# Kernel tuning notes

Hardware: AMD Instinct MI355X
Metric: run time of the kernel (lower is better)

The kernel has to match this reference:

```python
import jax, jax.numpy as jnp
import numpy as np

B, S, D = 2, 2048, 2048
H = 16
HD = D // H  # 128
ROPE_BASE = 10000.0


def _rope_cos_sin(seq_len, head_dim):
    inv_freq = 1.0 / (ROPE_BASE ** (jnp.arange(0, head_dim, 2, dtype=jnp.float32) / head_dim))
    t = jnp.arange(seq_len, dtype=jnp.float32)
    freqs = jnp.einsum('i,j->ij', t, inv_freq)  # [S, HD/2]
    emb = jnp.concatenate([freqs, freqs], axis=-1)  # [S, HD]
    return jnp.cos(emb)[None, None], jnp.sin(emb)[None, None]  # [1,1,S,HD]


def _rotate_half(x):
    x1, x2 = jnp.split(x, 2, axis=-1)
    return jnp.concatenate([-x2, x1], axis=-1)


def setup_inputs() -> dict:
    key = jax.random.key(0)
    k1, k2, k3 = jax.random.split(key, 3)
    hidden_states = jax.random.normal(k1, (B, S, D), dtype=jnp.float32)
    w_qkv = jax.random.normal(k2, (D, 3 * D), dtype=jnp.float32) * (D ** -0.5)
    w_o = jax.random.normal(k3, (D, D), dtype=jnp.float32) * (D ** -0.5)
    return {"hidden_states": hidden_states, "w_qkv": w_qkv, "w_o": w_o}


def reference(hidden_states, w_qkv, w_o):
    b, s, _ = hidden_states.shape
    qkv = jnp.einsum('bsd,de->bse', hidden_states, w_qkv)  # [B,S,3D]
    q, k, v = jnp.split(qkv, 3, axis=-1)
    # [B,H,S,HD]
    q = q.reshape(b, s, H, HD).transpose(0, 2, 1, 3)
    k = k.reshape(b, s, H, HD).transpose(0, 2, 1, 3)
    v = v.reshape(b, s, H, HD).transpose(0, 2, 1, 3)
    cos, sin = _rope_cos_sin(s, HD)
    q = q * cos + _rotate_half(q) * sin
    k = k * cos + _rotate_half(k) * sin
    scale = 1.0 / np.sqrt(HD).astype(np.float32)
    scores = jnp.einsum('bhqd,bhkd->bhqk', q, k) * scale  # [B,H,S,S]
    causal = jnp.triu(jnp.ones((s, s), dtype=bool), k=1)
    scores = jnp.where(causal, -jnp.inf, scores)
    attn = jax.nn.softmax(scores, axis=-1)
    out = jnp.einsum('bhqk,bhkd->bhqd', attn, v)  # [B,H,S,HD]
    out = out.transpose(0, 2, 1, 3).reshape(b, s, H * HD)
    return jnp.einsum('bsd,de->bse', out, w_o)
```

## Files before the change

kernel.cpp:

```cpp
#include <hip/hip_runtime.h>
#include <math.h>

typedef unsigned short u16;
typedef short s16x8 __attribute__((ext_vector_type(8)));
typedef float f32x4 __attribute__((ext_vector_type(4)));

#define ATTN_SCALE 0.08838834764831845f
#define NEG_BIG -1.0e30f

__device__ __forceinline__ u16 f2bf(float f) {
  union { float f; unsigned u; } c; c.f = f;
  return (u16)((c.u + 0x7fffu + ((c.u >> 16) & 1u)) >> 16);
}
__device__ __forceinline__ float bf2f(u16 v) {
  union { unsigned u; float f; } c; c.u = ((unsigned)v) << 16;
  return c.f;
}
__device__ __forceinline__ f32x4 mfma16(s16x8 a, s16x8 b, f32x4 c) {
  return __builtin_amdgcn_mfma_f32_16x16x32_bf16(a, b, c, 0, 0, 0);
}
__device__ __forceinline__ void gl_lds16(const u16* g, u16* l) {
  __builtin_amdgcn_global_load_lds(
      (const __attribute__((address_space(1))) unsigned int*)g,
      (__attribute__((address_space(3))) unsigned int*)l, 16, 0, 0);
}

__global__ __launch_bounds__(256) void k_cast(const float* __restrict__ in,
                                              u16* __restrict__ out, int n4) {
  const int i = blockIdx.x * 256 + threadIdx.x;
  if (i >= n4) return;
  const float4 v = ((const float4*)in)[i];
  ushort4 o;
  o.x = f2bf(v.x); o.y = f2bf(v.y); o.z = f2bf(v.z); o.w = f2bf(v.w);
  ((ushort4*)out)[i] = o;
}

__global__ __launch_bounds__(256) void k_transpose_cast(const float* __restrict__ in,
                                                        u16* __restrict__ out,
                                                        int R, int C) {
  __shared__ __attribute__((aligned(16))) u16 tile[32][33];
  const int c0 = blockIdx.x * 32, r0 = blockIdx.y * 32;
  const int tx = threadIdx.x, ty = threadIdx.y;
#pragma unroll
  for (int i = 0; i < 4; ++i)
    tile[ty + 8 * i][tx] = f2bf(in[(r0 + ty + 8 * i) * C + c0 + tx]);
  __syncthreads();
#pragma unroll
  for (int i = 0; i < 4; ++i)
    out[(c0 + ty + 8 * i) * R + r0 + tx] = tile[tx][ty + 8 * i];
}

__global__ __launch_bounds__(256) void k_vtrans(const u16* __restrict__ qkv,
                                                u16* __restrict__ vt) {
  __shared__ __attribute__((aligned(16))) u16 tile[32][33];
  const int bh = blockIdx.z, b = bh >> 4, h = bh & 15;
  const int s0 = blockIdx.x * 32, d0 = blockIdx.y * 32;
  const int tx = threadIdx.x, ty = threadIdx.y;
#pragma unroll
  for (int i = 0; i < 4; ++i) {
    const int s = s0 + ty + 8 * i;
    tile[ty + 8 * i][tx] = qkv[(b * 2048 + s) * 6144 + 4096 + h * 128 + d0 + tx];
  }
  __syncthreads();
#pragma unroll
  for (int i = 0; i < 4; ++i) {
    const int d = d0 + ty + 8 * i;
    vt[bh * 262144 + d * 2048 + s0 + tx] = tile[tx][ty + 8 * i];
  }
}

__global__ __launch_bounds__(256) void k_rope(u16* __restrict__ qkv) {
  const int id = blockIdx.x * 256 + threadIdx.x;
  const int j = id & 63;
  const int h = (id >> 6) & 15;
  const int sec = (id >> 10) & 1;
  const int m = id >> 11;
  const int s = m & 2047;
  const int base = m * 6144 + sec * 2048 + h * 128 + j;
  const float q0 = bf2f(qkv[base]);
  const float q1 = bf2f(qkv[base + 64]);
  const float inv = exp2f((float)j * -0.20762050593046014f);
  const float ang = (float)s * inv;
  float c, sn;
  sincosf(ang, &sn, &c);
  qkv[base]      = f2bf(q0 * c - q1 * sn);
  qkv[base + 64] = f2bf(q1 * c + q0 * sn);
}

template <bool A_F32, typename OUT_T>
__global__ __launch_bounds__(256) void k_gemm_lds(const void* __restrict__ Ap, int lda,
                                                  const u16* __restrict__ BT,
                                                  OUT_T* __restrict__ C, int ldc,
                                                  int K) {
  __shared__ __attribute__((aligned(16))) u16 As[128 * 32];
  __shared__ __attribute__((aligned(16))) u16 Bs[128 * 32];
  const int tid = threadIdx.x;
  const int lane = tid & 63, wave = tid >> 6;
  const int lm = lane & 15, quad = lane >> 4;
  const int wm = wave >> 1, wn = wave & 1;
  const int m0 = blockIdx.y * 128, n0 = blockIdx.x * 128;
  const int srow = lane >> 2, scol = (lane & 3) * 8;

  const f32x4 fzero = {0.f, 0.f, 0.f, 0.f};
  f32x4 acc[4][4];
#pragma unroll
  for (int i = 0; i < 4; ++i)
#pragma unroll
    for (int j = 0; j < 4; ++j) acc[i][j] = fzero;

  for (int k0 = 0; k0 < K; k0 += 32) {
    __syncthreads();
    if constexpr (A_F32) {
      const float* Af = (const float*)Ap;
#pragma unroll
      for (int i = 0; i < 2; ++i) {
        const int seg = tid + 256 * i;
        const int row = seg >> 2, c8 = (seg & 3) * 8;
        const float4 u = *(const float4*)&Af[(m0 + row) * lda + k0 + c8];
        const float4 w = *(const float4*)&Af[(m0 + row) * lda + k0 + c8 + 4];
        uint4 pk;
        pk.x = (unsigned)f2bf(u.x) | ((unsigned)f2bf(u.y) << 16);
        pk.y = (unsigned)f2bf(u.z) | ((unsigned)f2bf(u.w) << 16);
        pk.z = (unsigned)f2bf(w.x) | ((unsigned)f2bf(w.y) << 16);
        pk.w = (unsigned)f2bf(w.z) | ((unsigned)f2bf(w.w) << 16);
        *(uint4*)&As[row * 32 + c8] = pk;
      }
#pragma unroll
      for (int j = 0; j < 2; ++j) {
        const int rb = wave * 32 + j * 16;
        gl_lds16(&BT[(n0 + rb + srow) * K + k0 + scol], &Bs[rb * 32]);
      }
    } else {
      const u16* Ab = (const u16*)Ap;
#pragma unroll
      for (int j = 0; j < 2; ++j) {
        const int rb = wave * 32 + j * 16;
        gl_lds16(&Ab[(m0 + rb + srow) * lda + k0 + scol], &As[rb * 32]);
        gl_lds16(&BT[(n0 + rb + srow) * K + k0 + scol], &Bs[rb * 32]);
      }
    }
    __syncthreads();

    s16x8 af[4], bfr[4];
#pragma unroll
    for (int t = 0; t < 4; ++t) {
      af[t]  = *(const s16x8*)&As[(wm * 64 + t * 16 + lm) * 32 + quad * 8];
      bfr[t] = *(const s16x8*)&Bs[(wn * 64 + t * 16 + lm) * 32 + quad * 8];
    }
#pragma unroll
    for (int mt = 0; mt < 4; ++mt)
#pragma unroll
      for (int nt = 0; nt < 4; ++nt)
        acc[mt][nt] = mfma16(af[mt], bfr[nt], acc[mt][nt]);
  }
#pragma unroll
  for (int mt = 0; mt < 4; ++mt)
#pragma unroll
    for (int nt = 0; nt < 4; ++nt)
#pragma unroll
      for (int r = 0; r < 4; ++r) {
        const float v = acc[mt][nt][r];
        const int idx = (m0 + wm * 64 + mt * 16 + quad * 4 + r) * ldc +
                        n0 + wn * 64 + nt * 16 + lm;
        if constexpr (sizeof(OUT_T) == 2) C[idx] = f2bf(v);
        else                              C[idx] = v;
      }
}

__global__ __launch_bounds__(512, 2) void k_gemm256(const u16* __restrict__ A,
                                                    const u16* __restrict__ BT,
                                                    u16* __restrict__ C, int ldc) {
  __shared__ __attribute__((aligned(16))) u16 As[2][2][256 * 32];
  __shared__ __attribute__((aligned(16))) u16 Bs[2][2][256 * 32];
  const int K = 2048;
  const int tid = threadIdx.x;
  const int lane = tid & 63, wave = tid >> 6;
  const int lm = lane & 15, quad = lane >> 4;
  const int wm = wave >> 2, wn = wave & 3;

  int bid = (blockIdx.x & 7) * (gridDim.x >> 3) + (blockIdx.x >> 3);
  const int m0 = (bid & 15) * 256;
  const int n0 = (bid >> 4) * 256;

  auto stage_half = [&](int kt, int kc, int bi) {
    const int k0 = kt * 64 + kc * 32;
#pragma unroll
    for (int i = 0; i < 2; ++i) {
      const int r = i * 128 + 16 * wave + (lane >> 2);
      const int gc = (lane & 3) ^ (r & 3);
      gl_lds16(&A[(m0 + r) * K + k0 + gc * 8],
               &As[bi][kc][(i * 128 + 16 * wave) * 32]);
      gl_lds16(&BT[(n0 + r) * K + k0 + gc * 8],
               &Bs[bi][kc][(i * 128 + 16 * wave) * 32]);
    }
  };

  const f32x4 fzero = {0.f, 0.f, 0.f, 0.f};
  f32x4 acc[8][4];
#pragma unroll
  for (int i = 0; i < 8; ++i)
#pragma unroll
    for (int j = 0; j < 4; ++j) acc[i][j] = fzero;

  stage_half(0, 0, 0);
  stage_half(0, 1, 0);

  for (int t = 0; t < 32; ++t) {
    const int b = t & 1;
#pragma unroll
    for (int kc = 0; kc < 2; ++kc) {
      if (t == 31 && kc == 1) {
        asm volatile("s_waitcnt vmcnt(0)" ::: "memory");
      } else {
        asm volatile("s_waitcnt vmcnt(4)" ::: "memory");
      }
      asm volatile("s_barrier" ::: "memory");

      if (t < 31) stage_half(t + 1, kc, b ^ 1);

      s16x8 bfrag[4], afrag[8];
#pragma unroll
      for (int nt = 0; nt < 4; ++nt) {
        const int r = wn * 64 + nt * 16 + lm;
        const int cc = quad ^ (r & 3);
        bfrag[nt] = *(const s16x8*)&Bs[b][kc][r * 32 + cc * 8];
      }
#pragma unroll
      for (int mt = 0; mt < 8; ++mt) {
        const int r = wm * 128 + mt * 16 + lm;
        const int cc = quad ^ (r & 3);
        afrag[mt] = *(const s16x8*)&As[b][kc][r * 32 + cc * 8];
      }

      __builtin_amdgcn_s_setprio(1);
#pragma unroll
      for (int mt = 0; mt < 8; ++mt)
#pragma unroll
        for (int nt = 0; nt < 4; ++nt)
          acc[mt][nt] = mfma16(afrag[mt], bfrag[nt], acc[mt][nt]);
      __builtin_amdgcn_s_setprio(0);
    }
  }

#pragma unroll
  for (int mt = 0; mt < 8; ++mt)
#pragma unroll
    for (int nt = 0; nt < 4; ++nt)
#pragma unroll
      for (int r = 0; r < 4; ++r)
        C[(m0 + wm * 128 + mt * 16 + quad * 4 + r) * ldc +
          n0 + wn * 64 + nt * 16 + lm] = f2bf(acc[mt][nt][r]);
}

__global__ __launch_bounds__(256) void k_attn(u16* __restrict__ qkv,
                                              const u16* __restrict__ vt) {
  __shared__ __attribute__((aligned(16))) u16 Ks[2][64 * 128];
  __shared__ __attribute__((aligned(16))) u16 Vs[2][128 * 64];
  __shared__ __attribute__((aligned(16))) u16 Ps[4 * 16 * 72];
  const int bh = blockIdx.x, pair = blockIdx.y;
  const int b = bh >> 4, h = bh & 15;
  const int tid = threadIdx.x;
  const int lane = tid & 63, wave = tid >> 6;
  const int lm = lane & 15, quad = lane >> 4;
  const int pbase = wave * 1152;
  const int sw = lm & 7;
  const f32x4 fzero = {0.f, 0.f, 0.f, 0.f};

  const int phase_end = pair;

  auto dma_tile = [&](int kt0, int buf) {
#pragma unroll
    for (int i = 0; i < 4; ++i) {
      const int row = i * 16 + wave * 4 + (lane >> 4);
      const int cc = (lane & 15) ^ (row & 7);
      gl_lds16(&qkv[(b * 2048 + kt0 + row) * 6144 + 2048 + h * 128 + cc * 8],
               &Ks[buf][(i * 16 + wave * 4) * 128]);
    }
#pragma unroll
    for (int i = 0; i < 4; ++i) {
      const int row = i * 32 + wave * 8 + (lane >> 3);
      const int cc = (lane & 7) ^ (row & 7);
      gl_lds16(&vt[bh * 262144 + row * 2048 + kt0 + cc * 8],
               &Vs[buf][(i * 32 + wave * 8) * 64]);
    }
  };

  dma_tile(0, 0);

  int qtile = pair;
  int qb = qtile * 64;
  int qrow = qb + wave * 16 + lm;
  int qoff = (b * 2048 + qrow) * 6144 + h * 128;
  s16x8 qfrag[4];
#pragma unroll
  for (int c = 0; c < 4; ++c)
    qfrag[c] = *(const s16x8*)&qkv[qoff + c * 32 + quad * 8];
  f32x4 o[8];
#pragma unroll
  for (int dt = 0; dt < 8; ++dt) o[dt] = fzero;
  float m_run = NEG_BIG, l_run = 0.f;

  __syncthreads();

  for (int it = 0; it < 33; ++it) {
    const int kt0 = (it <= phase_end ? it : it - phase_end - 1) * 64;
    const int buf = it & 1;

    if (it < 32) {
      const int nkt = (it + 1 <= phase_end ? it + 1 : it - phase_end) * 64;
      dma_tile(nkt, buf ^ 1);
    }

    f32x4 sa[4];
#pragma unroll
    for (int ss = 0; ss < 4; ++ss) sa[ss] = fzero;
#pragma unroll
    for (int ss = 0; ss < 4; ++ss)
#pragma unroll
      for (int c = 0; c < 4; ++c) {
        const int ccs = (c * 4 + quad) ^ sw;
        s16x8 a = *(const s16x8*)&Ks[buf][(ss * 16 + lm) * 128 + ccs * 8];
        sa[ss] = mfma16(a, qfrag[c], sa[ss]);
      }

    float p[4][4];
    float vmax = NEG_BIG;
#pragma unroll
    for (int ss = 0; ss < 4; ++ss)
#pragma unroll
      for (int r = 0; r < 4; ++r) {
        const int kg = kt0 + ss * 16 + quad * 4 + r;
        float v = sa[ss][r] * ATTN_SCALE;
        if (kg > qrow) v = NEG_BIG;
        p[ss][r] = v;
        vmax = fmaxf(vmax, v);
      }
    vmax = fmaxf(vmax, __shfl_xor(vmax, 16, 64));
    vmax = fmaxf(vmax, __shfl_xor(vmax, 32, 64));
    const float m_new = fmaxf(m_run, vmax);
    const float alpha = __expf(m_run - m_new);
    float rsum = 0.f;
#pragma unroll
    for (int ss = 0; ss < 4; ++ss)
#pragma unroll
      for (int r = 0; r < 4; ++r) {
        p[ss][r] = __expf(p[ss][r] - m_new);
        rsum += p[ss][r];
      }
    rsum += __shfl_xor(rsum, 16, 64);
    rsum += __shfl_xor(rsum, 32, 64);
    l_run = l_run * alpha + rsum;
    m_run = m_new;
#pragma unroll
    for (int dt = 0; dt < 8; ++dt) o[dt] *= alpha;

#pragma unroll
    for (int ss = 0; ss < 4; ++ss)
#pragma unroll
      for (int r = 0; r < 4; ++r)
        Ps[pbase + lm * 72 + ss * 16 + quad * 4 + r] = f2bf(p[ss][r]);
    const s16x8 pv0 = *(const s16x8*)&Ps[pbase + lm * 72 + quad * 8];
    const s16x8 pv1 = *(const s16x8*)&Ps[pbase + lm * 72 + 32 + quad * 8];

#pragma unroll
    for (int dt = 0; dt < 8; ++dt) {
      const int c0 = (quad ^ sw) * 8, c1 = ((4 + quad) ^ sw) * 8;
      s16x8 a0 = *(const s16x8*)&Vs[buf][(dt * 16 + lm) * 64 + c0];
      s16x8 a1 = *(const s16x8*)&Vs[buf][(dt * 16 + lm) * 64 + c1];
      o[dt] = mfma16(a1, pv1, mfma16(a0, pv0, o[dt]));
    }

    if (it == phase_end) {
      const float inv_l = 1.0f / l_run;
#pragma unroll
      for (int dt = 0; dt < 8; ++dt)
#pragma unroll
        for (int r = 0; r < 4; ++r)
          qkv[qoff + dt * 16 + quad * 4 + r] = f2bf(o[dt][r] * inv_l);
      qtile = 31 - pair;
      qb = qtile * 64;
      qrow = qb + wave * 16 + lm;
      qoff = (b * 2048 + qrow) * 6144 + h * 128;
#pragma unroll
      for (int c = 0; c < 4; ++c)
        qfrag[c] = *(const s16x8*)&qkv[qoff + c * 32 + quad * 8];
#pragma unroll
      for (int dt = 0; dt < 8; ++dt) o[dt] = fzero;
      m_run = NEG_BIG; l_run = 0.f;
    }

    if (it < 32) __syncthreads();
  }

  const float inv_l = 1.0f / l_run;
#pragma unroll
  for (int dt = 0; dt < 8; ++dt)
#pragma unroll
    for (int r = 0; r < 4; ++r)
      qkv[qoff + dt * 16 + quad * 4 + r] = f2bf(o[dt][r] * inv_l);
}

extern "C" void kernel_launch(void* const* d_in, const int* in_sizes, int n_in,
                              void* d_out, int out_size, void* d_ws, size_t ws_size,
                              hipStream_t stream) {
  const float* hidden = (const float*)d_in[0];
  const float* w_qkv  = (const float*)d_in[1];
  const float* w_o    = (const float*)d_in[2];
  float* out = (float*)d_out;
  u16* ws = (u16*)d_ws;

  u16* qkv   = ws;
  u16* wqkvT = ws + 25165824;
  u16* vt    = ws + 25165824;
  u16* woT   = ws + 33554432;
  u16* hb    = ws + 37748736;
  const bool fast = ws_size >= (size_t)46137344 * 2;

  dim3 tb(32, 8);
  k_transpose_cast<<<dim3(192, 64), tb, 0, stream>>>(w_qkv, wqkvT, 2048, 6144);
  if (fast) {
    k_cast<<<8192, 256, 0, stream>>>(hidden, hb, 2097152);
    k_gemm256<<<384, 512, 0, stream>>>(hb, wqkvT, qkv, 6144);
  } else {
    k_gemm_lds<true, u16><<<dim3(48, 32), 256, 0, stream>>>(hidden, 2048, wqkvT,
                                                            qkv, 6144, 2048);
  }
  k_rope<<<32768, 256, 0, stream>>>(qkv);
  k_vtrans<<<dim3(64, 4, 32), tb, 0, stream>>>(qkv, vt);
  k_transpose_cast<<<dim3(64, 64), tb, 0, stream>>>(w_o, woT, 2048, 2048);
  k_attn<<<dim3(32, 16), 256, 0, stream>>>(qkv, vt);
  k_gemm_lds<false, float><<<dim3(16, 32), 256, 0, stream>>>(qkv, 6144, woT,
                                                             out, 2048, 2048);
}
```

Baseline: 454.6 us.

## Use triple-buffered 32-wide K units with prefetch distance two in GEMM

Replaces the double-buffered 64-wide K tiles in the 256x256 GEMM with a 3-slot ring of 32-wide K units, prefetched two units ahead. Fragments are read from LDS before the next unit's loads are issued, and a barrier separates the MFMA phase, so global-to-LDS copies overlap more compute. The LDS footprint drops from four half-tiles to three per operand. It adds an extra barrier per unit and more per-step loop overhead.

Measured after the change: 420.2 us. 7.6% less time.

```diff
diff --git a/kernel.cpp b/kernel.cpp
--- a/kernel.cpp
+++ b/kernel.cpp
@@ -170,8 +170,8 @@
 __global__ __launch_bounds__(512, 2) void k_gemm256(const u16* __restrict__ A,
                                                     const u16* __restrict__ BT,
                                                     u16* __restrict__ C, int ldc) {
-  __shared__ __attribute__((aligned(16))) u16 As[2][2][256 * 32];
-  __shared__ __attribute__((aligned(16))) u16 Bs[2][2][256 * 32];
+  __shared__ __attribute__((aligned(16))) u16 As[3][256 * 32];
+  __shared__ __attribute__((aligned(16))) u16 Bs[3][256 * 32];
   const int K = 2048;
   const int tid = threadIdx.x;
   const int lane = tid & 63, wave = tid >> 6;
@@ -182,16 +182,16 @@
   const int m0 = (bid & 15) * 256;
   const int n0 = (bid >> 4) * 256;
 
-  auto stage_half = [&](int kt, int kc, int bi) {
-    const int k0 = kt * 64 + kc * 32;
+  auto stage_unit = [&](int u, int bi) {
+    const int k0 = u * 32;
 #pragma unroll
     for (int i = 0; i < 2; ++i) {
       const int r = i * 128 + 16 * wave + (lane >> 2);
       const int gc = (lane & 3) ^ (r & 3);
       gl_lds16(&A[(m0 + r) * K + k0 + gc * 8],
-               &As[bi][kc][(i * 128 + 16 * wave) * 32]);
+               &As[bi][(i * 128 + 16 * wave) * 32]);
       gl_lds16(&BT[(n0 + r) * K + k0 + gc * 8],
-               &Bs[bi][kc][(i * 128 + 16 * wave) * 32]);
+               &Bs[bi][(i * 128 + 16 * wave) * 32]);
     }
   };
 
@@ -202,44 +202,47 @@
 #pragma unroll
     for (int j = 0; j < 4; ++j) acc[i][j] = fzero;
 
-  stage_half(0, 0, 0);
-  stage_half(0, 1, 0);
-
-  for (int t = 0; t < 32; ++t) {
-    const int b = t & 1;
-#pragma unroll
-    for (int kc = 0; kc < 2; ++kc) {
-      if (t == 31 && kc == 1) {
-        asm volatile("s_waitcnt vmcnt(0)" ::: "memory");
-      } else {
-        asm volatile("s_waitcnt vmcnt(4)" ::: "memory");
-      }
-      asm volatile("s_barrier" ::: "memory");
-
-      if (t < 31) stage_half(t + 1, kc, b ^ 1);
-
-      s16x8 bfrag[4], afrag[8];
-#pragma unroll
-      for (int nt = 0; nt < 4; ++nt) {
-        const int r = wn * 64 + nt * 16 + lm;
-        const int cc = quad ^ (r & 3);
-        bfrag[nt] = *(const s16x8*)&Bs[b][kc][r * 32 + cc * 8];
-      }
-#pragma unroll
-      for (int mt = 0; mt < 8; ++mt) {
-        const int r = wm * 128 + mt * 16 + lm;
-        const int cc = quad ^ (r & 3);
-        afrag[mt] = *(const s16x8*)&As[b][kc][r * 32 + cc * 8];
-      }
-
-      __builtin_amdgcn_s_setprio(1);
-#pragma unroll
-      for (int mt = 0; mt < 8; ++mt)
-#pragma unroll
-        for (int nt = 0; nt < 4; ++nt)
-          acc[mt][nt] = mfma16(afrag[mt], bfrag[nt], acc[mt][nt]);
-      __builtin_amdgcn_s_setprio(0);
-    }
+  stage_unit(0, 0);
+  stage_unit(1, 1);
+  asm volatile("s_waitcnt vmcnt(4)" ::: "memory");
+  __builtin_amdgcn_s_barrier();
+
+  int bi = 0;
+  for (int u = 0; u < 64; ++u) {
+    s16x8 bfrag[4], afrag[8];
+#pragma unroll
+    for (int nt = 0; nt < 4; ++nt) {
+      const int r = wn * 64 + nt * 16 + lm;
+      const int cc = quad ^ (r & 3);
+      bfrag[nt] = *(const s16x8*)&Bs[bi][r * 32 + cc * 8];
+    }
+#pragma unroll
+    for (int mt = 0; mt < 8; ++mt) {
+      const int r = wm * 128 + mt * 16 + lm;
+      const int cc = quad ^ (r & 3);
+      afrag[mt] = *(const s16x8*)&As[bi][r * 32 + cc * 8];
+    }
+    if (u < 62) {
+      int bi2 = bi + 2; if (bi2 >= 3) bi2 -= 3;
+      stage_unit(u + 2, bi2);
+    }
+
+    if (u < 62)       asm volatile("s_waitcnt vmcnt(4)" ::: "memory");
+    else if (u == 62) asm volatile("s_waitcnt vmcnt(0)" ::: "memory");
+    __builtin_amdgcn_s_barrier();
+    asm volatile("s_waitcnt lgkmcnt(0)" ::: "memory");
+    __builtin_amdgcn_sched_barrier(0);
+
+    __builtin_amdgcn_s_setprio(1);
+#pragma unroll
+    for (int mt = 0; mt < 8; ++mt)
+#pragma unroll
+      for (int nt = 0; nt < 4; ++nt)
+        acc[mt][nt] = mfma16(afrag[mt], bfrag[nt], acc[mt][nt]);
+    __builtin_amdgcn_s_setprio(0);
+    if (u < 63) __builtin_amdgcn_s_barrier();
+
+    bi = (bi == 2) ? 0 : bi + 1;
   }
 
 #pragma unroll
```

## Restructure GEMM main loop into quarter-step staging with split A fragments

Applied to the files above, without the earlier changes.

Rewrites the 256x256 GEMM main loop so each K-step is split into four quarters. Each quarter issues one A or B global-to-LDS load for the next tile, reads half of the A fragments, and runs a 4x4 block of MFMAs. The change aims to interleave loads with compute more finely and to lower fragment register pressure. It drops the XOR swizzle on the LDS layout and adds more barriers plus explicit lgkmcnt waits per quarter, which risks LDS bank conflicts and extra synchronisation cost.

Measured after the change: 416.1 us. 8.5% less time.

```diff
diff --git a/kernel.cpp b/kernel.cpp
--- a/kernel.cpp
+++ b/kernel.cpp
@@ -182,16 +182,17 @@
   const int m0 = (bid & 15) * 256;
   const int n0 = (bid >> 4) * 256;
 
-  auto stage_half = [&](int kt, int kc, int bi) {
-    const int k0 = kt * 64 + kc * 32;
-#pragma unroll
-    for (int i = 0; i < 2; ++i) {
-      const int r = i * 128 + 16 * wave + (lane >> 2);
-      const int gc = (lane & 3) ^ (r & 3);
-      gl_lds16(&A[(m0 + r) * K + k0 + gc * 8],
-               &As[bi][kc][(i * 128 + 16 * wave) * 32]);
-      gl_lds16(&BT[(n0 + r) * K + k0 + gc * 8],
-               &Bs[bi][kc][(i * 128 + 16 * wave) * 32]);
+  const int srow = lane >> 2, schunk = (lane & 3) * 8;
+  auto stage_q = [&](int t, int matA, int ks) {
+    const int buf = t & 1;
+    const int k0 = t * 64 + ks * 32 + schunk;
+    const u16* src = matA ? A : BT;
+    const int gb = matA ? m0 : n0;
+    u16* dst = matA ? &As[buf][ks][0] : &Bs[buf][ks][0];
+#pragma unroll
+    for (int j = 0; j < 2; ++j) {
+      const int r0 = j * 128 + wave * 16;
+      gl_lds16(&src[(gb + r0 + srow) * K + k0], dst + r0 * 32);
     }
   };
 
@@ -202,43 +203,41 @@
 #pragma unroll
     for (int j = 0; j < 4; ++j) acc[i][j] = fzero;
 
-  stage_half(0, 0, 0);
-  stage_half(0, 1, 0);
-
-  for (int t = 0; t < 32; ++t) {
-    const int b = t & 1;
-#pragma unroll
-    for (int kc = 0; kc < 2; ++kc) {
-      if (t == 31 && kc == 1) {
-        asm volatile("s_waitcnt vmcnt(0)" ::: "memory");
-      } else {
-        asm volatile("s_waitcnt vmcnt(4)" ::: "memory");
+  stage_q(0, 0, 0); stage_q(0, 1, 0); stage_q(0, 0, 1); stage_q(0, 1, 1);
+  asm volatile("s_waitcnt vmcnt(4)" ::: "memory");
+  asm volatile("s_barrier" ::: "memory");
+
+  s16x8 bfr[4], afr[4];
+  for (int c = 0; c < 32; ++c) {
+    const int buf = c & 1;
+#pragma unroll
+    for (int q = 0; q < 4; ++q) {
+      const int ks = q >> 1, mh = q & 1;
+      if (mh == 0) {
+#pragma unroll
+        for (int nt = 0; nt < 4; ++nt)
+          bfr[nt] = *(const s16x8*)
+              &Bs[buf][ks][(wn * 64 + nt * 16 + lm) * 32 + quad * 8];
+      }
+#pragma unroll
+      for (int i = 0; i < 4; ++i)
+        afr[i] = *(const s16x8*)
+            &As[buf][ks][(wm * 128 + mh * 64 + i * 16 + lm) * 32 + quad * 8];
+      if (c < 31) stage_q(c + 1, mh, ks);
+      if (mh == 1) {
+        if (c == 31) { asm volatile("s_waitcnt vmcnt(0)" ::: "memory"); }
+        else         { asm volatile("s_waitcnt vmcnt(4)" ::: "memory"); }
       }
       asm volatile("s_barrier" ::: "memory");
-
-      if (t < 31) stage_half(t + 1, kc, b ^ 1);
-
-      s16x8 bfrag[4], afrag[8];
-#pragma unroll
-      for (int nt = 0; nt < 4; ++nt) {
-        const int r = wn * 64 + nt * 16 + lm;
-        const int cc = quad ^ (r & 3);
-        bfrag[nt] = *(const s16x8*)&Bs[b][kc][r * 32 + cc * 8];
-      }
-#pragma unroll
-      for (int mt = 0; mt < 8; ++mt) {
-        const int r = wm * 128 + mt * 16 + lm;
-        const int cc = quad ^ (r & 3);
-        afrag[mt] = *(const s16x8*)&As[b][kc][r * 32 + cc * 8];
-      }
-
+      asm volatile("s_waitcnt lgkmcnt(0)" ::: "memory");
       __builtin_amdgcn_s_setprio(1);
 #pragma unroll
-      for (int mt = 0; mt < 8; ++mt)
+      for (int i = 0; i < 4; ++i)
 #pragma unroll
         for (int nt = 0; nt < 4; ++nt)
-          acc[mt][nt] = mfma16(afrag[mt], bfrag[nt], acc[mt][nt]);
+          acc[mh * 4 + i][nt] = mfma16(afr[i], bfr[nt], acc[mh * 4 + i][nt]);
       __builtin_amdgcn_s_setprio(0);
+      asm volatile("s_barrier" ::: "memory");
     }
   }
 
```
